# Performance work log

Measured on AMD Instinct MI355X. Metric: run time of the kernel, lower is better.

## Reference

```python
import jax, jax.numpy as jnp
import numpy as np
from jax import lax

EMB = 30
K = 5

def leaky(x):
    return jnp.where(x > 0, x, 0.1 * x)

def conv_resid(x, W, b):
    # x: [L, EMB]; W: [EMB, EMB, 3]; SAME trigram conv (matches torch pad=2 + slice) + residual
    y = lax.conv_general_dilated(x.T[None], W, window_strides=(1,), padding=[(1, 1)])  # [1,EMB,L]
    y = leaky(y + b[None, :, None])
    return y[0].T + x

def cosine_sim(A, B):
    num = A @ B.T                                   # [Qa, Qb]
    den = jnp.linalg.norm(A, axis=1)[:, None] * jnp.linalg.norm(B, axis=1)[None, :]
    return num / den

def kmax_pool(sim):
    top = lax.top_k(sim, K)[0]                      # [Q, K] descending
    return jnp.stack([top[:, 0], top.mean(axis=-1)], axis=-1)  # [Q, 2]

def get_output(pools, w, W1, W2):
    temp = jnp.concatenate(pools, axis=-1)          # [Q, 6]
    lo = leaky(temp @ W1.T) @ W2.T                  # [Q, 1]
    lo = lo[:, 0] * w
    return lo.sum() / lo.shape[0]

def setup_inputs() -> dict:
    key = jax.random.key(0)
    ks = jax.random.split(key, 12)
    Q, D = 2048, 8192
    inp = {
        "doc1_embeds": jax.random.normal(ks[0], (D, EMB), jnp.float32),
        "doc2_embeds": jax.random.normal(ks[1], (D, EMB), jnp.float32),
        "question_embeds": jax.random.normal(ks[2], (Q, EMB), jnp.float32),
        "q_idfs": jax.random.uniform(ks[3], (Q, 1), jnp.float32),
        "gaf": jax.random.uniform(ks[4], (4,), jnp.float32),
        "baf": jax.random.uniform(ks[5], (4,), jnp.float32),
        "W_conv": jax.random.normal(ks[6], (EMB, EMB, 3), jnp.float32) * 0.1,
        "b_conv": jax.random.normal(ks[7], (EMB,), jnp.float32) * 0.1,
        "W_qw": jax.random.normal(ks[8], (1, EMB + 1), jnp.float32) * 0.1,
        "W_q1": jax.random.normal(ks[9], (8, 6), jnp.float32) * 0.3,
        "W_q2": jax.random.normal(ks[10], (1, 8), jnp.float32) * 0.3,
        "W_out": jax.random.normal(ks[11], (1, 5), jnp.float32) * 0.3,
    }
    return inp

def reference(doc1_embeds, doc2_embeds, question_embeds, q_idfs, gaf, baf,
              W_conv, b_conv, W_qw, W_q1, W_q2, W_out):
    sim_i_d1 = cosine_sim(question_embeds, doc1_embeds)
    sim_i_d2 = cosine_sim(question_embeds, doc2_embeds)
    sim_oh_d1 = (sim_i_d1 > 1 - 0.001).astype(jnp.float32)
    sim_oh_d2 = (sim_i_d2 > 1 - 0.001).astype(jnp.float32)
    q_conv = conv_resid(question_embeds, W_conv, b_conv)
    d1_conv = conv_resid(doc1_embeds, W_conv, b_conv)
    d2_conv = conv_resid(doc2_embeds, W_conv, b_conv)
    sim_s_d1 = cosine_sim(q_conv, d1_conv)
    sim_s_d2 = cosine_sim(q_conv, d2_conv)
    q_weights = jax.nn.softmax((jnp.concatenate([q_conv, q_idfs], axis=-1) @ W_qw.T)[:, 0])
    doc1_emit = get_output([kmax_pool(sim_oh_d1), kmax_pool(sim_i_d1), kmax_pool(sim_s_d1)], q_weights, W_q1, W_q2)
    doc2_emit = get_output([kmax_pool(sim_oh_d2), kmax_pool(sim_i_d2), kmax_pool(sim_s_d2)], q_weights, W_q1, W_q2)
    good_out = jnp.concatenate([gaf, doc1_emit[None]]) @ W_out.T  # [1]
    bad_out = jnp.concatenate([baf, doc2_emit[None]]) @ W_out.T   # [1]
    loss1 = jnp.sum(jax.nn.relu(1.0 + bad_out - good_out), axis=-1)
    return (loss1, good_out, bad_out)
```

## Files before the change

kernel.cpp:

```cpp
#include <hip/hip_runtime.h>
#include <hip/hip_bf16.h>
#include <math.h>

#define EMB 30
#define NS 32
#define JT 256
#define SUB 64

typedef __attribute__((ext_vector_type(8))) short bf16x8;
typedef __attribute__((ext_vector_type(4))) float f32x4;
typedef __attribute__((ext_vector_type(4))) unsigned u32x4;
typedef __attribute__((ext_vector_type(2))) _Float16 f16x2;

__device__ __forceinline__ float leakyf(float x) { return x > 0.0f ? x : 0.1f * x; }

__device__ __forceinline__ unsigned short f2b(float x) {
  __hip_bfloat16 h = __float2bfloat16(x);
  union { __hip_bfloat16 h; unsigned short u; } cv;
  cv.h = h;
  return cv.u;
}

__device__ __forceinline__ unsigned pkmax(unsigned a, unsigned b) {
  unsigned d;
  asm("v_pk_max_f16 %0, %1, %2" : "=v"(d) : "v"(a), "v"(b));
  return d;
}
__device__ __forceinline__ unsigned pkmin(unsigned a, unsigned b) {
  unsigned d;
  asm("v_pk_min_f16 %0, %1, %2" : "=v"(d) : "v"(a), "v"(b));
  return d;
}
__device__ __forceinline__ unsigned cvtpku(float a, float b) {
  return __builtin_bit_cast(unsigned, __builtin_amdgcn_cvt_pkrtz(a, b));
}

__device__ __forceinline__ void ins5h(unsigned (&t)[5], unsigned v) {
  unsigned n0 = pkmax(t[0], v);
  unsigned n1 = pkmax(pkmin(t[0], v), t[1]);
  unsigned n2 = pkmax(pkmin(t[1], v), t[2]);
  unsigned n3 = pkmax(pkmin(t[2], v), t[3]);
  unsigned n4 = pkmax(pkmin(t[3], v), t[4]);
  t[0] = n0; t[1] = n1; t[2] = n2; t[3] = n3; t[4] = n4;
}

__device__ __forceinline__ void merge5h(unsigned (&a)[5], const unsigned (&b)[5]) {
  unsigned c0 = pkmax(a[0], b[0]);
  unsigned c1 = pkmax(pkmax(pkmin(a[0], b[0]), a[1]), b[1]);
  unsigned c2 = pkmax(pkmax(pkmin(a[0], b[1]), pkmin(a[1], b[0])), pkmax(a[2], b[2]));
  unsigned c3 = pkmax(pkmax(pkmin(a[0], b[2]), pkmin(a[1], b[1])),
                      pkmax(pkmin(a[2], b[0]), pkmax(a[3], b[3])));
  unsigned c4 = pkmax(pkmax(pkmax(pkmin(a[0], b[3]), pkmin(a[1], b[2])),
                            pkmax(pkmin(a[2], b[1]), pkmin(a[3], b[0]))),
                      pkmax(a[4], b[4]));
  a[0] = c0; a[1] = c1; a[2] = c2; a[3] = c3; a[4] = c4;
}

__device__ __forceinline__ void merge5(float (&a)[5], const float (&b)[5]) {
  float c0 = fmaxf(a[0], b[0]);
  float c1 = fmaxf(fmaxf(fminf(a[0], b[0]), a[1]), b[1]);
  float c2 = fmaxf(fmaxf(fminf(a[0], b[1]), fminf(a[1], b[0])), fmaxf(a[2], b[2]));
  float c3 = fmaxf(fmaxf(fminf(a[0], b[2]), fminf(a[1], b[1])),
                   fmaxf(fminf(a[2], b[0]), fmaxf(a[3], b[3])));
  float c4 = fmaxf(fmaxf(fmaxf(fminf(a[0], b[3]), fminf(a[1], b[2])),
                         fmaxf(fminf(a[2], b[1]), fminf(a[3], b[0]))),
                   fmaxf(a[4], b[4]));
  a[0] = c0; a[1] = c1; a[2] = c2; a[3] = c3; a[4] = c4;
}

template <int PAT>
__device__ __forceinline__ void bfly_round(unsigned (&t)[8][5]) {
#pragma unroll
  for (int li = 0; li < 8; ++li) {
    unsigned b[5];
#pragma unroll
    for (int k = 0; k < 5; ++k)
      b[k] = (unsigned)__builtin_amdgcn_ds_swizzle((int)t[li][k], PAT);
    merge5h(t[li], b);
  }
}

__global__ __launch_bounds__(256) void prep_all_kernel(
    const float* __restrict__ Xq, const float* __restrict__ X1,
    const float* __restrict__ X2, int Q, int D,
    const float* __restrict__ Wc, const float* __restrict__ bc,
    const float* __restrict__ qidf, const float* __restrict__ Wqw,
    unsigned short* __restrict__ qr, unsigned short* __restrict__ qc,
    unsigned short* __restrict__ cmb, float* __restrict__ logits) {
  __shared__ float sX[66 * EMB];
  __shared__ float sW[EMB * EMB * 3];
  __shared__ float sB[EMB];
  __shared__ float sQw[EMB + 1];
  int tid = threadIdx.x;
  int nbQ = Q >> 6, nbD = D >> 6;
  int b = blockIdx.x;
  const float* X;
  int L, l0, slot = 0;
  bool isQ = false;
  if (b < nbQ) { X = Xq; L = Q; l0 = b << 6; isQ = true; }
  else if (b < nbQ + nbD) { X = X1; L = D; l0 = (b - nbQ) << 6; slot = 0; }
  else { X = X2; L = D; l0 = (b - nbQ - nbD) << 6; slot = 2; }

  for (int idx = tid; idx < EMB * EMB * 3; idx += 256) sW[idx] = Wc[idx];
  if (tid < EMB) sB[tid] = bc[tid];
  if (tid < EMB + 1) sQw[tid] = Wqw[tid];
  int base = l0 * EMB - EMB;
  int lim = L * EMB;
  for (int idx = tid; idx < 66 * EMB; idx += 256) {
    int g = base + idx;
    sX[idx] = (g >= 0 && g < lim) ? X[g] : 0.0f;
  }
  __syncthreads();

  int r = tid >> 2, sub = tid & 3;
  int l = l0 + r;
  int o0 = sub * 8;
  const float* xmP = sX + r * EMB;
  const float* x0P = sX + (r + 1) * EMB;
  const float* xpP = sX + (r + 2) * EMB;
  const float* wP  = sW + o0 * 90;

  float acc[8];
#pragma unroll
  for (int oo = 0; oo < 8; ++oo)
    acc[oo] = (o0 + oo < EMB) ? sB[o0 + oo] : 0.0f;
  float sr = 0.0f;
  for (int i = 0; i < EMB; ++i) {
    float xm = xmP[i], x0v = x0P[i], xp = xpP[i];
    sr += x0v * x0v;
#pragma unroll
    for (int oo = 0; oo < 8; ++oo) {
      if (o0 + oo < EMB) {
        acc[oo] += wP[oo * 90 + i * 3 + 0] * xm;
        acc[oo] += wP[oo * 90 + i * 3 + 1] * x0v;
        acc[oo] += wP[oo * 90 + i * 3 + 2] * xp;
      }
    }
  }
  float y[8];
  float sc = 0.0f, lg = 0.0f;
#pragma unroll
  for (int oo = 0; oo < 8; ++oo) {
    if (o0 + oo < EMB) {
      float v = leakyf(acc[oo]) + x0P[o0 + oo];
      y[oo] = v;
      sc += v * v;
      lg += v * sQw[o0 + oo];
    } else y[oo] = 0.0f;
  }
  sc += __shfl_xor(sc, 1); sc += __shfl_xor(sc, 2);
  lg += __shfl_xor(lg, 1); lg += __shfl_xor(lg, 2);
  float rnr = 1.0f / sqrtf(sr);
  float rnc = 1.0f / sqrtf(sc);
  if (isQ && sub == 0) logits[l] = lg + qidf[l] * sQw[EMB];

  unsigned rd[4], cd[4];
#pragma unroll
  for (int kk = 0; kk < 4; ++kk) {
    int k = sub * 4 + kk;
    if (k < 15) {
      rd[kk] = (unsigned)f2b(x0P[2 * k] * rnr) | ((unsigned)f2b(x0P[2 * k + 1] * rnr) << 16);
      int oo = 2 * k - o0;
      cd[kk] = (unsigned)f2b(y[oo] * rnc) | ((unsigned)f2b(y[oo + 1] * rnc) << 16);
    } else { rd[kk] = 0u; cd[kk] = 0u; }
  }
  if (isQ) {
    unsigned* rw = (unsigned*)(qr + (size_t)l * 32);
    unsigned* cw = (unsigned*)(qc + (size_t)l * 32);
#pragma unroll
    for (int kk = 0; kk < 4; ++kk) { rw[sub * 4 + kk] = rd[kk]; cw[sub * 4 + kk] = cd[kk]; }
  } else {
    unsigned* rowp = (unsigned*)(cmb + (size_t)l * 128);
    int sx = (l & 7) << 2;
#pragma unroll
    for (int kk = 0; kk < 4; ++kk) {
      int k = sub * 4 + kk;
      rowp[(slot * 16 + k) ^ sx]       = rd[kk];
      rowp[((slot + 1) * 16 + k) ^ sx] = cd[kk];
    }
  }
}

__global__ __launch_bounds__(256) void main_kernel(
    const unsigned short* __restrict__ qrA, const unsigned short* __restrict__ qcA,
    const unsigned* __restrict__ cmb32,
    float* __restrict__ partials, int Q, int D) {
  __shared__ __align__(16) unsigned lds[2][SUB * 64];
  int tid = threadIdx.x;
  int wave = tid >> 6, lane = tid & 63;
  int lo = lane & 15, hi = lane >> 4;
  int qt = blockIdx.x >> 5, ds = blockIdx.x & (NS - 1);
  int qrow = qt * 64 + wave * 16 + lo;
  bf16x8 aR = *(const bf16x8*)(qrA + (size_t)qrow * 32 + hi * 8);
  bf16x8 aC = *(const bf16x8*)(qcA + (size_t)qrow * 32 + hi * 8);

  unsigned t[8][5];
#pragma unroll
  for (int li = 0; li < 8; ++li)
#pragma unroll
    for (int k = 0; k < 5; ++k) t[li][k] = 0xC000C000u;

  const u32x4* gsrc = (const u32x4*)(cmb32 + (size_t)ds * JT * 64);
  u32x4 R[4];
#pragma unroll
  for (int i = 0; i < 4; ++i) R[i] = gsrc[i * 256 + tid];
#pragma unroll
  for (int i = 0; i < 4; ++i) ((u32x4*)lds[0])[i * 256 + tid] = R[i];

  int swzA = ((lo & 7) << 2);
  int c0 = (0  + hi * 4) ^ swzA;
  int c1 = (16 + hi * 4) ^ swzA;
  int c2 = (32 + hi * 4) ^ swzA;
  int c3 = (48 + hi * 4) ^ swzA;

#pragma unroll 1
  for (int st = 0; st < 4; ++st) {
    __syncthreads();
    if (st < 3) {
#pragma unroll
      for (int i = 0; i < 4; ++i) R[i] = gsrc[(st + 1) * 1024 + i * 256 + tid];
    }
    const unsigned* L = lds[st & 1];
#pragma unroll
    for (int it = 0; it < 4; ++it) {
      const unsigned* rp = L + (it * 16 + lo) * 64;
      bf16x8 X0 = *(const bf16x8*)(rp + c0);
      bf16x8 X1 = *(const bf16x8*)(rp + c1);
      bf16x8 X2 = *(const bf16x8*)(rp + c2);
      bf16x8 X3 = *(const bf16x8*)(rp + c3);
      f32x4 z = {0.0f, 0.0f, 0.0f, 0.0f};
      f32x4 s0 = __builtin_amdgcn_mfma_f32_16x16x32_bf16(aR, X0, z, 0, 0, 0);
      f32x4 s1 = __builtin_amdgcn_mfma_f32_16x16x32_bf16(aC, X1, z, 0, 0, 0);
      f32x4 s2 = __builtin_amdgcn_mfma_f32_16x16x32_bf16(aR, X2, z, 0, 0, 0);
      f32x4 s3 = __builtin_amdgcn_mfma_f32_16x16x32_bf16(aC, X3, z, 0, 0, 0);
#pragma unroll
      for (int r = 0; r < 4; ++r) {
        ins5h(t[r * 2 + 0], cvtpku(s0[r], s2[r]));
        ins5h(t[r * 2 + 1], cvtpku(s1[r], s3[r]));
      }
    }
    __syncthreads();
    if (st < 3) {
#pragma unroll
      for (int i = 0; i < 4; ++i) ((u32x4*)lds[(st + 1) & 1])[i * 256 + tid] = R[i];
    }
  }

  bfly_round<0x041F>(t);
  bfly_round<0x081F>(t);
  bfly_round<0x101F>(t);
  bfly_round<0x201F>(t);

  if (lo == 0) {
#pragma unroll
    for (int r = 0; r < 4; ++r) {
      int q = qt * 64 + wave * 16 + hi * 4 + r;
      float* dst = partials + ((size_t)q * NS + ds) * 20;
#pragma unroll
      for (int k = 0; k < 5; ++k) {
        f16x2 t0 = __builtin_bit_cast(f16x2, t[r * 2 + 0][k]);
        f16x2 t1 = __builtin_bit_cast(f16x2, t[r * 2 + 1][k]);
        dst[k]      = (float)t0[0];
        dst[5 + k]  = (float)t1[0];
        dst[10 + k] = (float)t0[1];
        dst[15 + k] = (float)t1[1];
      }
    }
  }
}

__global__ __launch_bounds__(256) void pool_kernel(
    const float* __restrict__ logits, const float* __restrict__ partials,
    const float* __restrict__ W1, const float* __restrict__ W2,
    float* __restrict__ blockSums, int Q) {
  __shared__ float sred[4];
  __shared__ float sP[8 * 641];
  int tid = threadIdx.x;
  int lane = tid & 63, wave = tid >> 6;

  float lmax = -3.0e38f;
  for (int q = tid; q < Q; q += 256) lmax = fmaxf(lmax, logits[q]);
#pragma unroll
  for (int m = 1; m < 64; m <<= 1) lmax = fmaxf(lmax, __shfl_xor(lmax, m));
  if (lane == 0) sred[wave] = lmax;
  __syncthreads();
  float M = fmaxf(fmaxf(sred[0], sred[1]), fmaxf(sred[2], sred[3]));
  __syncthreads();
  float lsum = 0.0f;
  for (int q = tid; q < Q; q += 256) lsum += expf(logits[q] - M);
#pragma unroll
  for (int m = 1; m < 64; m <<= 1) lsum += __shfl_xor(lsum, m);
  if (lane == 0) sred[wave] = lsum;
  __syncthreads();
  float rS = 1.0f / (sred[0] + sred[1] + sred[2] + sred[3]);

  size_t base = (size_t)blockIdx.x * 8 * NS * 20;
  for (int k = tid; k < 8 * NS * 20; k += 256) {
    int ql = k / 640, r = k - ql * 640;
    sP[ql * 641 + r] = partials[base + k];
  }
  __syncthreads();

  int ql = tid >> 5, dsp = tid & 31;
  int qglob = blockIdx.x * 8 + ql;
  float T[4][5];
#pragma unroll
  for (int li = 0; li < 4; ++li)
#pragma unroll
    for (int k = 0; k < 5; ++k) T[li][k] = sP[ql * 641 + dsp * 20 + li * 5 + k];
#pragma unroll
  for (int m = 16; m >= 1; m >>= 1) {
#pragma unroll
    for (int li = 0; li < 4; ++li) {
      float b[5];
#pragma unroll
      for (int k = 0; k < 5; ++k) b[k] = __shfl_xor(T[li][k], m);
      merge5(T[li], b);
    }
  }
  float s1 = 0.0f, s2 = 0.0f;
  if (dsp == 0) {
    float w = expf(logits[qglob] - M) * rS;
#pragma unroll
    for (int d = 0; d < 2; ++d) {
      const float (&Ti)[5] = T[d ? 2 : 0];
      const float (&Ts)[5] = T[d ? 3 : 1];
      float c = 0.0f;
#pragma unroll
      for (int k = 0; k < 5; ++k) c += (Ti[k] > 0.999f) ? 1.0f : 0.0f;
      float tmp[6];
      tmp[0] = (Ti[0] > 0.999f) ? 1.0f : 0.0f;
      tmp[1] = c * 0.2f;
      tmp[2] = Ti[0];
      tmp[3] = (Ti[0] + Ti[1] + Ti[2] + Ti[3] + Ti[4]) * 0.2f;
      tmp[4] = Ts[0];
      tmp[5] = (Ts[0] + Ts[1] + Ts[2] + Ts[3] + Ts[4]) * 0.2f;
      float lov = 0.0f;
#pragma unroll
      for (int r = 0; r < 8; ++r) {
        float h = 0.0f;
#pragma unroll
        for (int cidx = 0; cidx < 6; ++cidx) h += W1[r * 6 + cidx] * tmp[cidx];
        lov += W2[r] * leakyf(h);
      }
      if (d == 0) s1 = lov * w; else s2 = lov * w;
    }
  }
  __shared__ float r1[4], r2[4];
#pragma unroll
  for (int m = 1; m < 64; m <<= 1) { s1 += __shfl_xor(s1, m); s2 += __shfl_xor(s2, m); }
  if (lane == 0) { r1[wave] = s1; r2[wave] = s2; }
  __syncthreads();
  if (tid == 0) {
    blockSums[blockIdx.x * 2]     = r1[0] + r1[1] + r1[2] + r1[3];
    blockSums[blockIdx.x * 2 + 1] = r2[0] + r2[1] + r2[2] + r2[3];
  }
}

__global__ __launch_bounds__(64) void final_kernel(
    const float* __restrict__ blockSums, int nBlocks,
    const float* __restrict__ gaf, const float* __restrict__ baf,
    const float* __restrict__ Wout, float* __restrict__ out, int Q) {
  int tid = threadIdx.x;
  float s1 = 0.0f, s2 = 0.0f;
  for (int b = tid; b < nBlocks; b += 64) {
    s1 += blockSums[b * 2];
    s2 += blockSums[b * 2 + 1];
  }
#pragma unroll
  for (int m = 1; m < 64; m <<= 1) { s1 += __shfl_xor(s1, m); s2 += __shfl_xor(s2, m); }
  if (tid == 0) {
    float e1 = s1 / (float)Q, e2 = s2 / (float)Q;
    float good = gaf[0] * Wout[0] + gaf[1] * Wout[1] + gaf[2] * Wout[2] + gaf[3] * Wout[3] + e1 * Wout[4];
    float bad  = baf[0] * Wout[0] + baf[1] * Wout[1] + baf[2] * Wout[2] + baf[3] * Wout[3] + e2 * Wout[4];
    float loss = fmaxf(0.0f, 1.0f + bad - good);
    out[0] = loss; out[1] = good; out[2] = bad;
  }
}

extern "C" void kernel_launch(void* const* d_in, const int* in_sizes, int n_in,
                              void* d_out, int out_size, void* d_ws, size_t ws_size,
                              hipStream_t stream) {
  const float* d1   = (const float*)d_in[0];
  const float* d2   = (const float*)d_in[1];
  const float* qe   = (const float*)d_in[2];
  const float* qidf = (const float*)d_in[3];
  const float* gaf  = (const float*)d_in[4];
  const float* baf  = (const float*)d_in[5];
  const float* Wc   = (const float*)d_in[6];
  const float* bc   = (const float*)d_in[7];
  const float* Wqw  = (const float*)d_in[8];
  const float* Wq1  = (const float*)d_in[9];
  const float* Wq2  = (const float*)d_in[10];
  const float* Wout = (const float*)d_in[11];
  int D = in_sizes[0] / EMB;
  int Q = in_sizes[2] / EMB;

  unsigned short* us = (unsigned short*)d_ws;
  unsigned short* cmb = us; us += (size_t)D * 128;
  unsigned short* qrA = us; us += (size_t)Q * 32;
  unsigned short* qcA = us; us += (size_t)Q * 32;
  float* fp = (float*)us;
  float* logits    = fp; fp += Q;
  float* partials  = fp; fp += (size_t)Q * NS * 20;
  float* blockSums = fp; fp += (Q / 8) * 2;

  int grid = (Q >> 6) + 2 * (D >> 6);
  prep_all_kernel<<<grid, 256, 0, stream>>>(qe, d1, d2, Q, D, Wc, bc, qidf, Wqw,
                                            qrA, qcA, cmb, logits);
  main_kernel<<<(Q / 64) * NS, 256, 0, stream>>>(qrA, qcA, (const unsigned*)cmb,
                                                 partials, Q, D);
  pool_kernel<<<Q / 8, 256, 0, stream>>>(logits, partials, Wq1, Wq2, blockSums, Q);
  final_kernel<<<1, 64, 0, stream>>>(blockSums, Q / 8, gaf, baf, Wout, (float*)d_out, Q);
}
```

Measured before the change: 57.41 us.

## Load doc B-operands directly from global into registers, dropping LDS staging

The main kernel no longer stages doc tiles through double-buffered shared memory with barriers. Each wave now loads its MFMA B fragments straight from global memory with a two-deep register prefetch, and the XOR swizzle in the prep kernel's doc layout is removed to match. Launch bounds gain a minimum of four blocks per CU. This removes LDS traffic and the syncthreads, but each of the four waves in a block now reads the same doc data from global memory or cache, so L2 and VMEM traffic goes up.

```diff
diff --git a/kernel.cpp b/kernel.cpp
--- a/kernel.cpp
+++ b/kernel.cpp
@@ -5,11 +5,9 @@
 #define EMB 30
 #define NS 32
 #define JT 256
-#define SUB 64
 
 typedef __attribute__((ext_vector_type(8))) short bf16x8;
 typedef __attribute__((ext_vector_type(4))) float f32x4;
-typedef __attribute__((ext_vector_type(4))) unsigned u32x4;
 typedef __attribute__((ext_vector_type(2))) _Float16 f16x2;
 
 __device__ __forceinline__ float leakyf(float x) { return x > 0.0f ? x : 0.1f * x; }
@@ -171,28 +169,26 @@
     for (int kk = 0; kk < 4; ++kk) { rw[sub * 4 + kk] = rd[kk]; cw[sub * 4 + kk] = cd[kk]; }
   } else {
     unsigned* rowp = (unsigned*)(cmb + (size_t)l * 128);
-    int sx = (l & 7) << 2;
 #pragma unroll
     for (int kk = 0; kk < 4; ++kk) {
       int k = sub * 4 + kk;
-      rowp[(slot * 16 + k) ^ sx]       = rd[kk];
-      rowp[((slot + 1) * 16 + k) ^ sx] = cd[kk];
-    }
-  }
-}
-
-__global__ __launch_bounds__(256) void main_kernel(
+      rowp[slot * 16 + k]       = rd[kk];
+      rowp[(slot + 1) * 16 + k] = cd[kk];
+    }
+  }
+}
+
+__global__ __launch_bounds__(256, 4) void main_kernel(
     const unsigned short* __restrict__ qrA, const unsigned short* __restrict__ qcA,
-    const unsigned* __restrict__ cmb32,
+    const unsigned short* __restrict__ cmb,
     float* __restrict__ partials, int Q, int D) {
-  __shared__ __align__(16) unsigned lds[2][SUB * 64];
   int tid = threadIdx.x;
   int wave = tid >> 6, lane = tid & 63;
   int lo = lane & 15, hi = lane >> 4;
-  int qt = blockIdx.x >> 5, ds = blockIdx.x & (NS - 1);
-  int qrow = qt * 64 + wave * 16 + lo;
-  bf16x8 aR = *(const bf16x8*)(qrA + (size_t)qrow * 32 + hi * 8);
-  bf16x8 aC = *(const bf16x8*)(qcA + (size_t)qrow * 32 + hi * 8);
+  int qg = blockIdx.x >> 5, ds = blockIdx.x & (NS - 1);
+  int qbase = (qg * 4 + wave) * 16;
+  bf16x8 aR = *(const bf16x8*)(qrA + (size_t)(qbase + lo) * 32 + hi * 8);
+  bf16x8 aC = *(const bf16x8*)(qcA + (size_t)(qbase + lo) * 32 + hi * 8);
 
   unsigned t[8][5];
 #pragma unroll
@@ -200,49 +196,34 @@
 #pragma unroll
     for (int k = 0; k < 5; ++k) t[li][k] = 0xC000C000u;
 
-  const u32x4* gsrc = (const u32x4*)(cmb32 + (size_t)ds * JT * 64);
-  u32x4 R[4];
-#pragma unroll
-  for (int i = 0; i < 4; ++i) R[i] = gsrc[i * 256 + tid];
-#pragma unroll
-  for (int i = 0; i < 4; ++i) ((u32x4*)lds[0])[i * 256 + tid] = R[i];
-
-  int swzA = ((lo & 7) << 2);
-  int c0 = (0  + hi * 4) ^ swzA;
-  int c1 = (16 + hi * 4) ^ swzA;
-  int c2 = (32 + hi * 4) ^ swzA;
-  int c3 = (48 + hi * 4) ^ swzA;
-
-#pragma unroll 1
-  for (int st = 0; st < 4; ++st) {
-    __syncthreads();
-    if (st < 3) {
-#pragma unroll
-      for (int i = 0; i < 4; ++i) R[i] = gsrc[(st + 1) * 1024 + i * 256 + tid];
-    }
-    const unsigned* L = lds[st & 1];
-#pragma unroll
-    for (int it = 0; it < 4; ++it) {
-      const unsigned* rp = L + (it * 16 + lo) * 64;
-      bf16x8 X0 = *(const bf16x8*)(rp + c0);
-      bf16x8 X1 = *(const bf16x8*)(rp + c1);
-      bf16x8 X2 = *(const bf16x8*)(rp + c2);
-      bf16x8 X3 = *(const bf16x8*)(rp + c3);
-      f32x4 z = {0.0f, 0.0f, 0.0f, 0.0f};
-      f32x4 s0 = __builtin_amdgcn_mfma_f32_16x16x32_bf16(aR, X0, z, 0, 0, 0);
-      f32x4 s1 = __builtin_amdgcn_mfma_f32_16x16x32_bf16(aC, X1, z, 0, 0, 0);
-      f32x4 s2 = __builtin_amdgcn_mfma_f32_16x16x32_bf16(aR, X2, z, 0, 0, 0);
-      f32x4 s3 = __builtin_amdgcn_mfma_f32_16x16x32_bf16(aC, X3, z, 0, 0, 0);
-#pragma unroll
-      for (int r = 0; r < 4; ++r) {
-        ins5h(t[r * 2 + 0], cvtpku(s0[r], s2[r]));
-        ins5h(t[r * 2 + 1], cvtpku(s1[r], s3[r]));
-      }
-    }
-    __syncthreads();
-    if (st < 3) {
-#pragma unroll
-      for (int i = 0; i < 4; ++i) ((u32x4*)lds[(st + 1) & 1])[i * 256 + tid] = R[i];
+  const unsigned short* p = cmb + (size_t)(ds * JT + lo) * 128 + hi * 8;
+  bf16x8 B[2][4];
+#pragma unroll
+  for (int pre = 0; pre < 2; ++pre) {
+    const unsigned short* pp = p + pre * 2048;
+    B[pre][0] = *(const bf16x8*)(pp);
+    B[pre][1] = *(const bf16x8*)(pp + 32);
+    B[pre][2] = *(const bf16x8*)(pp + 64);
+    B[pre][3] = *(const bf16x8*)(pp + 96);
+  }
+#pragma unroll
+  for (int it = 0; it < 16; ++it) {
+    f32x4 z = {0.0f, 0.0f, 0.0f, 0.0f};
+    f32x4 s0 = __builtin_amdgcn_mfma_f32_16x16x32_bf16(aR, B[it & 1][0], z, 0, 0, 0);
+    f32x4 s1 = __builtin_amdgcn_mfma_f32_16x16x32_bf16(aC, B[it & 1][1], z, 0, 0, 0);
+    f32x4 s2 = __builtin_amdgcn_mfma_f32_16x16x32_bf16(aR, B[it & 1][2], z, 0, 0, 0);
+    f32x4 s3 = __builtin_amdgcn_mfma_f32_16x16x32_bf16(aC, B[it & 1][3], z, 0, 0, 0);
+    if (it + 2 < 16) {
+      const unsigned short* pp = p + (it + 2) * 2048;
+      B[it & 1][0] = *(const bf16x8*)(pp);
+      B[it & 1][1] = *(const bf16x8*)(pp + 32);
+      B[it & 1][2] = *(const bf16x8*)(pp + 64);
+      B[it & 1][3] = *(const bf16x8*)(pp + 96);
+    }
+#pragma unroll
+    for (int r = 0; r < 4; ++r) {
+      ins5h(t[r * 2 + 0], cvtpku(s0[r], s2[r]));
+      ins5h(t[r * 2 + 1], cvtpku(s1[r], s3[r]));
     }
   }
 
@@ -254,7 +235,7 @@
   if (lo == 0) {
 #pragma unroll
     for (int r = 0; r < 4; ++r) {
-      int q = qt * 64 + wave * 16 + hi * 4 + r;
+      int q = qbase + hi * 4 + r;
       float* dst = partials + ((size_t)q * NS + ds) * 20;
 #pragma unroll
       for (int k = 0; k < 5; ++k) {
@@ -408,8 +389,7 @@
   int grid = (Q >> 6) + 2 * (D >> 6);
   prep_all_kernel<<<grid, 256, 0, stream>>>(qe, d1, d2, Q, D, Wc, bc, qidf, Wqw,
                                             qrA, qcA, cmb, logits);
-  main_kernel<<<(Q / 64) * NS, 256, 0, stream>>>(qrA, qcA, (const unsigned*)cmb,
-                                                 partials, Q, D);
+  main_kernel<<<(Q / 64) * NS, 256, 0, stream>>>(qrA, qcA, cmb, partials, Q, D);
   pool_kernel<<<Q / 8, 256, 0, stream>>>(logits, partials, Wq1, Wq2, blockSums, Q);
   final_kernel<<<1, 64, 0, stream>>>(blockSums, Q / 8, gaf, baf, Wout, (float*)d_out, Q);
 }
```

Result: slower. 70.52 us (+22.8%).

## Retile main kernel: 128 queries per block, swap MFMA operands, split docs finer

Applied to the files above, without the earlier changes.

Each block now covers 128 query rows (32 per wave) against a 128-row document slice, with NS doubled to 64 splits. The MFMA operands are swapped so documents map to lanes' row dimension and queries to columns, which changes the top-5 cross-lane reduction from four ds_swizzle rounds to one swizzle plus one xor-32 shuffle. The aim is to reuse each loaded document tile across two query sub-tiles and shorten the cross-lane merge. In exchange, the partials buffer doubles and the pool kernel must merge 64 splits per query, with one wave per query.

```diff
diff --git a/kernel.cpp b/kernel.cpp
--- a/kernel.cpp
+++ b/kernel.cpp
@@ -3,8 +3,8 @@
 #include <math.h>
 
 #define EMB 30
-#define NS 32
-#define JT 256
+#define NS 64
+#define JT 128
 #define SUB 64
 
 typedef __attribute__((ext_vector_type(8))) short bf16x8;
@@ -66,18 +66,6 @@
                          fmaxf(fminf(a[2], b[1]), fminf(a[3], b[0]))),
                    fmaxf(a[4], b[4]));
   a[0] = c0; a[1] = c1; a[2] = c2; a[3] = c3; a[4] = c4;
-}
-
-template <int PAT>
-__device__ __forceinline__ void bfly_round(unsigned (&t)[8][5]) {
-#pragma unroll
-  for (int li = 0; li < 8; ++li) {
-    unsigned b[5];
-#pragma unroll
-    for (int k = 0; k < 5; ++k)
-      b[k] = (unsigned)__builtin_amdgcn_ds_swizzle((int)t[li][k], PAT);
-    merge5h(t[li], b);
-  }
 }
 
 __global__ __launch_bounds__(256) void prep_all_kernel(
@@ -181,7 +169,7 @@
   }
 }
 
-__global__ __launch_bounds__(256) void main_kernel(
+__global__ __launch_bounds__(256, 4) void main_kernel(
     const unsigned short* __restrict__ qrA, const unsigned short* __restrict__ qcA,
     const unsigned* __restrict__ cmb32,
     float* __restrict__ partials, int Q, int D) {
@@ -189,14 +177,16 @@
   int tid = threadIdx.x;
   int wave = tid >> 6, lane = tid & 63;
   int lo = lane & 15, hi = lane >> 4;
-  int qt = blockIdx.x >> 5, ds = blockIdx.x & (NS - 1);
-  int qrow = qt * 64 + wave * 16 + lo;
-  bf16x8 aR = *(const bf16x8*)(qrA + (size_t)qrow * 32 + hi * 8);
-  bf16x8 aC = *(const bf16x8*)(qcA + (size_t)qrow * 32 + hi * 8);
-
-  unsigned t[8][5];
-#pragma unroll
-  for (int li = 0; li < 8; ++li)
+  int qt = blockIdx.x >> 6, ds = blockIdx.x & (NS - 1);
+  int qb0 = qt * 128 + wave * 32;
+  bf16x8 aR0 = *(const bf16x8*)(qrA + (size_t)(qb0 + lo) * 32 + hi * 8);
+  bf16x8 aC0 = *(const bf16x8*)(qcA + (size_t)(qb0 + lo) * 32 + hi * 8);
+  bf16x8 aR1 = *(const bf16x8*)(qrA + (size_t)(qb0 + 16 + lo) * 32 + hi * 8);
+  bf16x8 aC1 = *(const bf16x8*)(qcA + (size_t)(qb0 + 16 + lo) * 32 + hi * 8);
+
+  unsigned t[4][5];
+#pragma unroll
+  for (int li = 0; li < 4; ++li)
 #pragma unroll
     for (int k = 0; k < 5; ++k) t[li][k] = 0xC000C000u;
 
@@ -214,13 +204,13 @@
   int c3 = (48 + hi * 4) ^ swzA;
 
 #pragma unroll 1
-  for (int st = 0; st < 4; ++st) {
+  for (int st = 0; st < 2; ++st) {
     __syncthreads();
-    if (st < 3) {
-#pragma unroll
-      for (int i = 0; i < 4; ++i) R[i] = gsrc[(st + 1) * 1024 + i * 256 + tid];
-    }
-    const unsigned* L = lds[st & 1];
+    if (st == 0) {
+#pragma unroll
+      for (int i = 0; i < 4; ++i) R[i] = gsrc[1024 + i * 256 + tid];
+    }
+    const unsigned* L = lds[st];
 #pragma unroll
     for (int it = 0; it < 4; ++it) {
       const unsigned* rp = L + (it * 16 + lo) * 64;
@@ -229,37 +219,54 @@
       bf16x8 X2 = *(const bf16x8*)(rp + c2);
       bf16x8 X3 = *(const bf16x8*)(rp + c3);
       f32x4 z = {0.0f, 0.0f, 0.0f, 0.0f};
-      f32x4 s0 = __builtin_amdgcn_mfma_f32_16x16x32_bf16(aR, X0, z, 0, 0, 0);
-      f32x4 s1 = __builtin_amdgcn_mfma_f32_16x16x32_bf16(aC, X1, z, 0, 0, 0);
-      f32x4 s2 = __builtin_amdgcn_mfma_f32_16x16x32_bf16(aR, X2, z, 0, 0, 0);
-      f32x4 s3 = __builtin_amdgcn_mfma_f32_16x16x32_bf16(aC, X3, z, 0, 0, 0);
+      f32x4 s0a = __builtin_amdgcn_mfma_f32_16x16x32_bf16(X0, aR0, z, 0, 0, 0);
+      f32x4 s1a = __builtin_amdgcn_mfma_f32_16x16x32_bf16(X1, aC0, z, 0, 0, 0);
+      f32x4 s2a = __builtin_amdgcn_mfma_f32_16x16x32_bf16(X2, aR0, z, 0, 0, 0);
+      f32x4 s3a = __builtin_amdgcn_mfma_f32_16x16x32_bf16(X3, aC0, z, 0, 0, 0);
+      f32x4 s0b = __builtin_amdgcn_mfma_f32_16x16x32_bf16(X0, aR1, z, 0, 0, 0);
+      f32x4 s1b = __builtin_amdgcn_mfma_f32_16x16x32_bf16(X1, aC1, z, 0, 0, 0);
+      f32x4 s2b = __builtin_amdgcn_mfma_f32_16x16x32_bf16(X2, aR1, z, 0, 0, 0);
+      f32x4 s3b = __builtin_amdgcn_mfma_f32_16x16x32_bf16(X3, aC1, z, 0, 0, 0);
 #pragma unroll
       for (int r = 0; r < 4; ++r) {
-        ins5h(t[r * 2 + 0], cvtpku(s0[r], s2[r]));
-        ins5h(t[r * 2 + 1], cvtpku(s1[r], s3[r]));
+        ins5h(t[0], cvtpku(s0a[r], s2a[r]));
+        ins5h(t[1], cvtpku(s1a[r], s3a[r]));
+        ins5h(t[2], cvtpku(s0b[r], s2b[r]));
+        ins5h(t[3], cvtpku(s1b[r], s3b[r]));
       }
     }
     __syncthreads();
-    if (st < 3) {
-#pragma unroll
-      for (int i = 0; i < 4; ++i) ((u32x4*)lds[(st + 1) & 1])[i * 256 + tid] = R[i];
-    }
-  }
-
-  bfly_round<0x041F>(t);
-  bfly_round<0x081F>(t);
-  bfly_round<0x101F>(t);
-  bfly_round<0x201F>(t);
-
-  if (lo == 0) {
-#pragma unroll
-    for (int r = 0; r < 4; ++r) {
-      int q = qt * 64 + wave * 16 + hi * 4 + r;
+    if (st == 0) {
+#pragma unroll
+      for (int i = 0; i < 4; ++i) ((u32x4*)lds[1])[i * 256 + tid] = R[i];
+    }
+  }
+
+#pragma unroll
+  for (int li = 0; li < 4; ++li) {
+    unsigned b[5];
+#pragma unroll
+    for (int k = 0; k < 5; ++k)
+      b[k] = (unsigned)__builtin_amdgcn_ds_swizzle((int)t[li][k], 0x401F);
+    merge5h(t[li], b);
+  }
+#pragma unroll
+  for (int li = 0; li < 4; ++li) {
+    unsigned b[5];
+#pragma unroll
+    for (int k = 0; k < 5; ++k) b[k] = (unsigned)__shfl_xor((int)t[li][k], 32);
+    merge5h(t[li], b);
+  }
+
+  if (lane < 16) {
+#pragma unroll
+    for (int qs = 0; qs < 2; ++qs) {
+      int q = qb0 + qs * 16 + lo;
       float* dst = partials + ((size_t)q * NS + ds) * 20;
 #pragma unroll
       for (int k = 0; k < 5; ++k) {
-        f16x2 t0 = __builtin_bit_cast(f16x2, t[r * 2 + 0][k]);
-        f16x2 t1 = __builtin_bit_cast(f16x2, t[r * 2 + 1][k]);
+        f16x2 t0 = __builtin_bit_cast(f16x2, t[qs * 2 + 0][k]);
+        f16x2 t1 = __builtin_bit_cast(f16x2, t[qs * 2 + 1][k]);
         dst[k]      = (float)t0[0];
         dst[5 + k]  = (float)t1[0];
         dst[10 + k] = (float)t0[1];
@@ -274,7 +281,8 @@
     const float* __restrict__ W1, const float* __restrict__ W2,
     float* __restrict__ blockSums, int Q) {
   __shared__ float sred[4];
-  __shared__ float sP[8 * 641];
+  __shared__ float sP[4 * 1281];
+  __shared__ float r1[4], r2[4];
   int tid = threadIdx.x;
   int lane = tid & 63, wave = tid >> 6;
 
@@ -294,22 +302,22 @@
   __syncthreads();
   float rS = 1.0f / (sred[0] + sred[1] + sred[2] + sred[3]);
 
-  size_t base = (size_t)blockIdx.x * 8 * NS * 20;
-  for (int k = tid; k < 8 * NS * 20; k += 256) {
-    int ql = k / 640, r = k - ql * 640;
-    sP[ql * 641 + r] = partials[base + k];
-  }
-  __syncthreads();
-
-  int ql = tid >> 5, dsp = tid & 31;
-  int qglob = blockIdx.x * 8 + ql;
+  size_t base = (size_t)blockIdx.x * 4 * NS * 20;
+  for (int k = tid; k < 4 * NS * 20; k += 256) {
+    int ql = k / 1280, r = k - ql * 1280;
+    sP[ql * 1281 + r] = partials[base + k];
+  }
+  __syncthreads();
+
+  int ql = wave, dsp = lane;
+  int qglob = blockIdx.x * 4 + ql;
   float T[4][5];
 #pragma unroll
   for (int li = 0; li < 4; ++li)
 #pragma unroll
-    for (int k = 0; k < 5; ++k) T[li][k] = sP[ql * 641 + dsp * 20 + li * 5 + k];
-#pragma unroll
-  for (int m = 16; m >= 1; m >>= 1) {
+    for (int k = 0; k < 5; ++k) T[li][k] = sP[ql * 1281 + dsp * 20 + li * 5 + k];
+#pragma unroll
+  for (int m = 32; m >= 1; m >>= 1) {
 #pragma unroll
     for (int li = 0; li < 4; ++li) {
       float b[5];
@@ -318,9 +326,9 @@
       merge5(T[li], b);
     }
   }
-  float s1 = 0.0f, s2 = 0.0f;
   if (dsp == 0) {
     float w = expf(logits[qglob] - M) * rS;
+    float s1 = 0.0f, s2 = 0.0f;
 #pragma unroll
     for (int d = 0; d < 2; ++d) {
       const float (&Ti)[5] = T[d ? 2 : 0];
@@ -345,11 +353,8 @@
       }
       if (d == 0) s1 = lov * w; else s2 = lov * w;
     }
-  }
-  __shared__ float r1[4], r2[4];
-#pragma unroll
-  for (int m = 1; m < 64; m <<= 1) { s1 += __shfl_xor(s1, m); s2 += __shfl_xor(s2, m); }
-  if (lane == 0) { r1[wave] = s1; r2[wave] = s2; }
+    r1[ql] = s1; r2[ql] = s2;
+  }
   __syncthreads();
   if (tid == 0) {
     blockSums[blockIdx.x * 2]     = r1[0] + r1[1] + r1[2] + r1[3];
@@ -403,13 +408,13 @@
   float* fp = (float*)us;
   float* logits    = fp; fp += Q;
   float* partials  = fp; fp += (size_t)Q * NS * 20;
-  float* blockSums = fp; fp += (Q / 8) * 2;
+  float* blockSums = fp; fp += (Q / 4) * 2;
 
   int grid = (Q >> 6) + 2 * (D >> 6);
   prep_all_kernel<<<grid, 256, 0, stream>>>(qe, d1, d2, Q, D, Wc, bc, qidf, Wqw,
                                             qrA, qcA, cmb, logits);
-  main_kernel<<<(Q / 64) * NS, 256, 0, stream>>>(qrA, qcA, (const unsigned*)cmb,
-                                                 partials, Q, D);
-  pool_kernel<<<Q / 8, 256, 0, stream>>>(logits, partials, Wq1, Wq2, blockSums, Q);
-  final_kernel<<<1, 64, 0, stream>>>(blockSums, Q / 8, gaf, baf, Wout, (float*)d_out, Q);
-}
+  main_kernel<<<(Q / 128) * NS, 256, 0, stream>>>(qrA, qcA, (const unsigned*)cmb,
+                                                  partials, Q, D);
+  pool_kernel<<<Q / 4, 256, 0, stream>>>(logits, partials, Wq1, Wq2, blockSums, Q);
+  final_kernel<<<1, 64, 0, stream>>>(blockSums, Q / 4, gaf, baf, Wout, (float*)d_out, Q);
+}
```

Result: faster. 56.12 us (-2.2%).
